# Kernel optimization log

Hardware: AMD Instinct MI355X
Metric: run time of the kernel (lower is better)

## Reference

```python
import jax, jax.numpy as jnp
import numpy as np

NUM_HEADS = 12
HEAD_DIM = 64
MASKED_BIAS = -10000.0


def setup_inputs() -> dict:
    key = jax.random.key(0)
    k1, k2, k3 = jax.random.split(key, 3)
    B, S, D = 2, 2048, 768
    return {
        "hidden_states": jax.random.normal(k1, (B, S, D), dtype=jnp.float32),
        "c_attn_w": jax.random.normal(k2, (D, 3 * D), dtype=jnp.float32) * 0.02,
        "c_attn_b": jnp.zeros((3 * D,), dtype=jnp.float32),
        "c_proj_w": jax.random.normal(k3, (D, D), dtype=jnp.float32) * 0.02,
        "c_proj_b": jnp.zeros((D,), dtype=jnp.float32),
    }


def _split_heads(x, B, S):
    # [B,S,D] -> [B,H,S,hd]
    return x.reshape(B, S, NUM_HEADS, HEAD_DIM).transpose(0, 2, 1, 3)


def reference(hidden_states, c_attn_w, c_attn_b, c_proj_w, c_proj_b):
    B, S, D = hidden_states.shape
    qkv = hidden_states @ c_attn_w + c_attn_b  # [B,S,3D]
    q, k, v = jnp.split(qkv, 3, axis=-1)
    q = _split_heads(q, B, S)
    k = _split_heads(k, B, S)
    v = _split_heads(v, B, S)

    # Unfused attention: full [B,H,S,S] scores, where-based causal mask
    attn_weights = jnp.einsum("bhqd,bhkd->bhqk", q, k)
    attn_weights = attn_weights / jnp.float32(HEAD_DIM) ** 0.5
    causal_mask = jnp.tril(jnp.ones((S, S), dtype=bool))[None, None]
    attn_weights = jnp.where(causal_mask, attn_weights,
                             jnp.asarray(MASKED_BIAS, attn_weights.dtype))
    attn_weights = jax.nn.softmax(attn_weights, axis=-1)
    attn_output = jnp.einsum("bhqk,bhkd->bhqd", attn_weights, v)

    # merge heads [B,H,S,hd] -> [B,S,D]
    attn_output = attn_output.transpose(0, 2, 1, 3).reshape(B, S, D)
    attn_output = attn_output @ c_proj_w + c_proj_b
    return attn_output
```

## Files before the change

### kernel.cpp

```cpp
#include <hip/hip_runtime.h>
#include <stdint.h>


constexpr int B_  = 2;
constexpr int S_  = 2048;
constexpr int D_  = 768;
constexpr int N3D = 3 * D_;
constexpr int M_  = B_ * S_;
constexpr int NTILE = 32 * 24;
#define QSCALE 0.1803368801111f
#define FIXED_M 8.0f

typedef __bf16 bv8 __attribute__((ext_vector_type(8)));
typedef float  fv4 __attribute__((ext_vector_type(4)));
typedef unsigned short uv4 __attribute__((ext_vector_type(4)));
typedef unsigned short uv8 __attribute__((ext_vector_type(8)));

__device__ inline unsigned short f2bf(float x) {
    __bf16 b = (__bf16)x;
    return __builtin_bit_cast(unsigned short, b);
}

__device__ inline fv4 mfma16(bv8 a, bv8 b, fv4 c) {
    return __builtin_amdgcn_mfma_f32_16x16x32_bf16(a, b, c, 0, 0, 0);
}

#define GLOAD_LDS16(g, l)                                                        \
    __builtin_amdgcn_global_load_lds(                                            \
        (__attribute__((address_space(1))) void*)(g),                            \
        (__attribute__((address_space(3))) void*)(l), 16, 0, 0)

#define VMCNT4() asm volatile("s_waitcnt vmcnt(4)" ::: "memory")
#define VMCNT0() asm volatile("s_waitcnt vmcnt(0)" ::: "memory")
#define BAR()                                                                    \
    do { asm volatile("" ::: "memory"); __builtin_amdgcn_s_barrier();            \
         asm volatile("" ::: "memory"); } while (0)

__global__ __launch_bounds__(256)
void prep(const float* __restrict__ hs, const float* __restrict__ wqkv,
          const float* __restrict__ wproj, unsigned short* __restrict__ hsb,
          unsigned short* __restrict__ wqkvT, unsigned short* __restrict__ wprojT,
          int* __restrict__ cnt)
{
    __shared__ float tl[32][33];
    const int bid = blockIdx.x, t = threadIdx.x;
    if (bid == 0 && t == 0) *cnt = 0;

    if (bid < 1536) {
        const size_t i = ((size_t)bid * 256 + t) * 8;
        const float4 a = *(const float4*)&hs[i];
        const float4 b = *(const float4*)&hs[i + 4];
        uv8 o;
        o[0] = f2bf(a.x); o[1] = f2bf(a.y); o[2] = f2bf(a.z); o[3] = f2bf(a.w);
        o[4] = f2bf(b.x); o[5] = f2bf(b.y); o[6] = f2bf(b.z); o[7] = f2bf(b.w);
        *(uv8*)&hsb[i] = o;
        return;
    }

    const float* W;
    unsigned short* WT;
    int K, N, bx, by;
    if (bid < 3264) {
        W = wqkv; WT = wqkvT; K = 768; N = 2304;
        const int b2 = bid - 1536; bx = b2 % 72; by = b2 / 72;
    } else {
        W = wproj; WT = wprojT; K = 768; N = 768;
        const int b2 = bid - 3264; bx = b2 % 24; by = b2 / 24;
    }
    const int n0 = bx * 32, k0 = by * 32;
    {
        const int r = t >> 3, c = (t & 7) * 4;
        const float4 v = *(const float4*)&W[(size_t)(k0 + r) * N + n0 + c];
        tl[r][c + 0] = v.x; tl[r][c + 1] = v.y; tl[r][c + 2] = v.z; tl[r][c + 3] = v.w;
    }
    __syncthreads();
    {
        const int rn = t >> 3, ck = (t & 7) * 4;
        uv4 o;
        o[0] = f2bf(tl[ck + 0][rn]); o[1] = f2bf(tl[ck + 1][rn]);
        o[2] = f2bf(tl[ck + 2][rn]); o[3] = f2bf(tl[ck + 3][rn]);
        *(uv4*)&WT[(size_t)(n0 + rn) * K + k0 + ck] = o;
    }
}

template<bool QKV>
__global__ __launch_bounds__(256)
void gemm_bf16(const unsigned short* __restrict__ A, const unsigned short* __restrict__ BT,
               const float* __restrict__ bias, float* __restrict__ Cf,
               unsigned short* __restrict__ Qb, unsigned short* __restrict__ Kb,
               unsigned short* __restrict__ VTb, int M, int N, int K)
{
    __shared__ unsigned short smem[16384];
    unsigned short* const sA0 = smem;
    unsigned short* const sB0 = smem + 8192;

    const int t = threadIdx.x, w = t >> 6, lane = t & 63;
    const int l15 = lane & 15, l4 = lane >> 4;
    const int m0 = blockIdx.y * 128, n0 = blockIdx.x * 128;
    const int wr = w >> 1, wc = w & 1;

    fv4 acc[4][4];
#pragma unroll
    for (int i = 0; i < 4; ++i)
#pragma unroll
        for (int j = 0; j < 4; ++j) acc[i][j] = fv4{0.f, 0.f, 0.f, 0.f};

    const int r0 = w * 16 + (lane >> 2);
    const int c0 = (lane & 3) ^ ((r0 >> 1) & 3);
    const int r1 = (w + 4) * 16 + (lane >> 2);
    const int c1 = (lane & 3) ^ ((r1 >> 1) & 3);

    auto stage = [&](int buf, int k0) {
        GLOAD_LDS16(A  + (size_t)(m0 + r0) * K + k0 + c0 * 8, sA0 + buf * 4096 + w * 512);
        GLOAD_LDS16(A  + (size_t)(m0 + r1) * K + k0 + c1 * 8, sA0 + buf * 4096 + (w + 4) * 512);
        GLOAD_LDS16(BT + (size_t)(n0 + r0) * K + k0 + c0 * 8, sB0 + buf * 4096 + w * 512);
        GLOAD_LDS16(BT + (size_t)(n0 + r1) * K + k0 + c1 * 8, sB0 + buf * 4096 + (w + 4) * 512);
    };

    stage(0, 0);
    const int nt = K >> 5;
    for (int tt = 0; tt < nt; ++tt) {
        const int cur = tt & 1;
        if (tt + 1 < nt) { stage(cur ^ 1, (tt + 1) * 32); VMCNT4(); }
        else             { VMCNT0(); }
        BAR();

        bv8 af[4], bf[4];
#pragma unroll
        for (int i = 0; i < 4; ++i) {
            const int r = wr * 64 + i * 16 + l15;
            const int c = l4 ^ ((r >> 1) & 3);
            af[i] = *(const bv8*)&sA0[cur * 4096 + r * 32 + c * 8];
        }
#pragma unroll
        for (int j = 0; j < 4; ++j) {
            const int r = wc * 64 + j * 16 + l15;
            const int c = l4 ^ ((r >> 1) & 3);
            bf[j] = *(const bv8*)&sB0[cur * 4096 + r * 32 + c * 8];
        }
        __builtin_amdgcn_s_setprio(1);
#pragma unroll
        for (int i = 0; i < 4; ++i)
#pragma unroll
            for (int j = 0; j < 4; ++j)
                acc[i][j] = mfma16(af[i], bf[j], acc[i][j]);
        __builtin_amdgcn_s_setprio(0);
        BAR();
    }

    if (QKV) {
        const int sect = n0 / 768;
        const int rem0 = n0 - sect * 768;
        if (sect < 2) {
            const float qs = (sect == 0) ? QSCALE : 1.0f;
#pragma unroll
            for (int jf = 0; jf < 4; ++jf) {
                const int c = wc * 64 + jf * 16 + l15;
                const float bb = bias[n0 + c];
                const int ch = c >> 3, off = c & 7;
#pragma unroll
                for (int i = 0; i < 4; ++i) {
                    const int rb = wr * 64 + i * 16 + l4 * 4;
#pragma unroll
                    for (int reg = 0; reg < 4; ++reg) {
                        const int r = rb + reg;
                        smem[r * 128 + ((ch ^ (r & 15)) << 3) + off] =
                            f2bf((acc[i][jf][reg] + bb) * qs);
                    }
                }
            }
            __syncthreads();
            unsigned short* const dstQK = (sect == 0) ? Qb : Kb;
            const int brow = m0 >> 11, sbase = m0 & 2047, hb = rem0 >> 6;
#pragma unroll
            for (int u = 0; u < 8; ++u) {
                const int ID = t + 256 * u;
                const int s = ID >> 4, ch = ID & 15;
                const int hh = ch >> 3, dc = ch & 7;
                const uv8 v = *(const uv8*)&smem[s * 128 + ((ch ^ (s & 15)) << 3)];
                const size_t bh = (size_t)brow * 12 + hb + hh;
                *(uv8*)&dstQK[(bh * 2048 + sbase + s) * 64 + dc * 8] = v;
            }
        } else {
#pragma unroll
            for (int jf = 0; jf < 4; ++jf) {
                const int col = n0 + wc * 64 + jf * 16 + l15;
                const float bb = bias[col];
                const int rem = col - 2 * 768;
                const int hh_ = rem >> 6, d = rem & 63;
#pragma unroll
                for (int i = 0; i < 4; ++i) {
                    const int rowb = m0 + wr * 64 + i * 16 + l4 * 4;
                    const size_t bh = (size_t)(rowb >> 11) * 12 + hh_;
                    const int s0 = rowb & 2047;
                    uv4 pk;
#pragma unroll
                    for (int reg = 0; reg < 4; ++reg) pk[reg] = f2bf(acc[i][jf][reg] + bb);
                    *(uv4*)&VTb[(bh * 64 + d) * 2048 + s0] = pk;
                }
            }
        }
    } else {
#pragma unroll
        for (int jf = 0; jf < 4; ++jf) {
            const int col = n0 + wc * 64 + jf * 16 + l15;
            const float bb = bias[col];
#pragma unroll
            for (int i = 0; i < 4; ++i) {
                const int rowb = m0 + wr * 64 + i * 16 + l4 * 4;
#pragma unroll
                for (int reg = 0; reg < 4; ++reg)
                    Cf[(size_t)(rowb + reg) * N + col] = acc[i][jf][reg] + bb;
            }
        }
    }
}

__global__ __launch_bounds__(256)
void flash_mfma(const unsigned short* __restrict__ Qb, const unsigned short* __restrict__ Kb,
                const unsigned short* __restrict__ VTb, unsigned short* __restrict__ outb,
                int* __restrict__ cnt)
{
    __shared__ unsigned short sK [2][64 * 64];
    __shared__ unsigned short sVT[2][64 * 64];
    __shared__ unsigned short sP [4][16 * 64];
    __shared__ int sj;

    const int t = threadIdx.x, w = t >> 6, lane = t & 63;
    const int l15 = lane & 15, l4 = lane >> 4;

    const int sr0 = w * 8 + (lane >> 3), sc0 = (lane & 7) ^ (sr0 & 7);
    const int sr1 = (w + 4) * 8 + (lane >> 3), sc1 = (lane & 7) ^ (sr1 & 7);

    for (;;) {
        if (t == 0) sj = atomicAdd(cnt, 1);
        __syncthreads();
        const int j = sj;
        if (j >= NTILE) return;
        const int qt = 31 - j / 24;
        const int bh = j - (j / 24) * 24;
        const int b = bh / 12, h = bh - b * 12;
        const int qrow = qt * 64 + w * 16;

        const unsigned short* Kbase = Kb  + (size_t)bh * 2048 * 64;
        const unsigned short* Vbase = VTb + (size_t)bh * 64 * 2048;

        bv8 qf[2];
        {
            const unsigned short* qp = Qb + ((size_t)bh * 2048 + qrow + l15) * 64 + l4 * 8;
            qf[0] = *(const bv8*)qp;
            qf[1] = *(const bv8*)(qp + 32);
        }

        fv4 o[4];
#pragma unroll
        for (int jf = 0; jf < 4; ++jf) o[jf] = fv4{0.f, 0.f, 0.f, 0.f};
        float l_ = 0.f;

        GLOAD_LDS16(Kbase + (size_t)sr0 * 64 + sc0 * 8, &sK[0][w * 512]);
        GLOAD_LDS16(Kbase + (size_t)sr1 * 64 + sc1 * 8, &sK[0][(w + 4) * 512]);
        GLOAD_LDS16(Vbase + (size_t)sr0 * 2048 + sc0 * 8, &sVT[0][w * 512]);
        GLOAD_LDS16(Vbase + (size_t)sr1 * 2048 + sc1 * 8, &sVT[0][(w + 4) * 512]);

        for (int kt = 0; kt <= qt; ++kt) {
            const int cur = kt & 1;
            if (kt < qt) {
                const int nk = kt + 1;
                GLOAD_LDS16(Kbase + (size_t)(nk * 64 + sr0) * 64 + sc0 * 8, &sK[cur ^ 1][w * 512]);
                GLOAD_LDS16(Kbase + (size_t)(nk * 64 + sr1) * 64 + sc1 * 8, &sK[cur ^ 1][(w + 4) * 512]);
                GLOAD_LDS16(Vbase + (size_t)sr0 * 2048 + nk * 64 + sc0 * 8, &sVT[cur ^ 1][w * 512]);
                GLOAD_LDS16(Vbase + (size_t)sr1 * 2048 + nk * 64 + sc1 * 8, &sVT[cur ^ 1][(w + 4) * 512]);
                VMCNT4();
            } else VMCNT0();
            BAR();

            fv4 st[4];
            __builtin_amdgcn_s_setprio(1);
#pragma unroll
            for (int jf = 0; jf < 4; ++jf) {
                st[jf] = fv4{-FIXED_M, -FIXED_M, -FIXED_M, -FIXED_M};
                const int kr = jf * 16 + l15;
#pragma unroll
                for (int hh = 0; hh < 2; ++hh) {
                    const bv8 ka = *(const bv8*)&sK[cur][kr * 64 + (((hh * 4 + l4) ^ (kr & 7)) * 8)];
                    st[jf] = mfma16(ka, qf[hh], st[jf]);
                }
            }
            __builtin_amdgcn_s_setprio(0);

            float ps[16];
            const int qg = qrow + l15;
            if (kt == qt) {
#pragma unroll
                for (int jf = 0; jf < 4; ++jf)
#pragma unroll
                    for (int reg = 0; reg < 4; ++reg) {
                        const int kvg = kt * 64 + jf * 16 + l4 * 4 + reg;
                        ps[jf * 4 + reg] = (kvg > qg) ? -30000.f : st[jf][reg];
                    }
            } else {
#pragma unroll
                for (int jf = 0; jf < 4; ++jf)
#pragma unroll
                    for (int reg = 0; reg < 4; ++reg) ps[jf * 4 + reg] = st[jf][reg];
            }
#pragma unroll
            for (int u = 0; u < 16; ++u) {
                const float p = exp2f(ps[u]);
                ps[u] = p;
                l_ += p;
            }

#pragma unroll
            for (int jf = 0; jf < 4; ++jf) {
                uv4 pk;
#pragma unroll
                for (int reg = 0; reg < 4; ++reg) pk[reg] = f2bf(ps[jf * 4 + reg]);
                const int chunk = jf * 2 + (l4 >> 1);
                *(uv4*)&sP[w][l15 * 64 + ((chunk ^ (l15 & 7)) * 8) + (l4 & 1) * 4] = pk;
            }

            bv8 pa[2];
#pragma unroll
            for (int hh = 0; hh < 2; ++hh)
                pa[hh] = *(const bv8*)&sP[w][l15 * 64 + (((hh * 4 + l4) ^ (l15 & 7)) * 8)];
            __builtin_amdgcn_s_setprio(1);
#pragma unroll
            for (int jf = 0; jf < 4; ++jf) {
                const int dr = jf * 16 + l15;
#pragma unroll
                for (int hh = 0; hh < 2; ++hh) {
                    const bv8 vb = *(const bv8*)&sVT[cur][dr * 64 + (((hh * 4 + l4) ^ (dr & 7)) * 8)];
                    o[jf] = mfma16(pa[hh], vb, o[jf]);
                }
            }
            __builtin_amdgcn_s_setprio(0);
            BAR();
        }

        l_ += __shfl_xor(l_, 16);
        l_ += __shfl_xor(l_, 32);
        const float inv = 1.0f / l_;
        float invq[4];
#pragma unroll
        for (int reg = 0; reg < 4; ++reg) invq[reg] = __shfl(inv, l4 * 4 + reg);
#pragma unroll
        for (int jf = 0; jf < 4; ++jf)
#pragma unroll
            for (int reg = 0; reg < 4; ++reg)
                outb[(size_t)(b * S_ + qrow + l4 * 4 + reg) * D_ + h * 64 + jf * 16 + l15] =
                    f2bf(o[jf][reg] * invq[reg]);
    }
}

extern "C" void kernel_launch(void* const* d_in, const int* in_sizes, int n_in,
                              void* d_out, int out_size, void* d_ws, size_t ws_size,
                              hipStream_t stream)
{
    const float* hs    = (const float*)d_in[0];
    const float* wqkv  = (const float*)d_in[1];
    const float* bqkv  = (const float*)d_in[2];
    const float* wproj = (const float*)d_in[3];
    const float* bproj = (const float*)d_in[4];
    float* out = (float*)d_out;

    unsigned short* hsb    = (unsigned short*)d_ws;
    unsigned short* wqkvT  = hsb    + (size_t)M_ * D_;
    unsigned short* wprojT = wqkvT  + (size_t)N3D * D_;
    unsigned short* Qb     = wprojT + (size_t)D_ * D_;
    unsigned short* Kb     = Qb     + (size_t)24 * 2048 * 64;
    unsigned short* VTb    = Kb     + (size_t)24 * 2048 * 64;
    unsigned short* attnb  = VTb    + (size_t)24 * 2048 * 64;
    int* cnt = (int*)(attnb + (size_t)M_ * D_);

    prep<<<3840, 256, 0, stream>>>(hs, wqkv, wproj, hsb, wqkvT, wprojT, cnt);
    gemm_bf16<true><<<dim3(N3D / 128, M_ / 128), 256, 0, stream>>>(
        hsb, wqkvT, bqkv, nullptr, Qb, Kb, VTb, M_, N3D, D_);
    flash_mfma<<<512, 256, 0, stream>>>(Qb, Kb, VTb, attnb, cnt);
    gemm_bf16<false><<<dim3(D_ / 128, M_ / 128), 256, 0, stream>>>(
        attnb, wprojT, bproj, out, nullptr, nullptr, nullptr, M_, D_, D_);
}
```

Measured before the change: 170.9 us.

## Split long causal attention tiles across two workgroups and triple-buffer GEMM loads

Query tiles 16-31 are split into two KV ranges handled by separate workgroups. The partial O and l values are combined through a global scratch buffer that reuses the hs bf16 region, using an atomic flag handshake with spin-wait. The change also moves the QKV/proj GEMMs to a 3-stage LDS pipeline, raises the flash grid from 512 to 768 persistent blocks, and splits the exp-sum into four accumulators. The aim is to balance the uneven causal workload and hide GEMM load latency, at the cost of more LDS per block, extra scratch traffic and a spin-wait that could stall if the partner block is not resident.

```diff
diff --git a/kernel.cpp b/kernel.cpp
--- a/kernel.cpp
+++ b/kernel.cpp
@@ -7,7 +7,7 @@
 constexpr int D_  = 768;
 constexpr int N3D = 3 * D_;
 constexpr int M_  = B_ * S_;
-constexpr int NTILE = 32 * 24;
+constexpr int NCHUNK = 1152;
 #define QSCALE 0.1803368801111f
 #define FIXED_M 8.0f
 
@@ -30,6 +30,7 @@
         (__attribute__((address_space(1))) void*)(g),                            \
         (__attribute__((address_space(3))) void*)(l), 16, 0, 0)
 
+#define VMCNT8() asm volatile("s_waitcnt vmcnt(8)" ::: "memory")
 #define VMCNT4() asm volatile("s_waitcnt vmcnt(4)" ::: "memory")
 #define VMCNT0() asm volatile("s_waitcnt vmcnt(0)" ::: "memory")
 #define BAR()                                                                    \
@@ -44,7 +45,9 @@
 {
     __shared__ float tl[32][33];
     const int bid = blockIdx.x, t = threadIdx.x;
-    if (bid == 0 && t == 0) *cnt = 0;
+    if (bid == 0) {
+        for (int i = t; i < 388; i += 256) cnt[i] = 0;
+    }
 
     if (bid < 1536) {
         const size_t i = ((size_t)bid * 256 + t) * 8;
@@ -90,9 +93,9 @@
                unsigned short* __restrict__ Qb, unsigned short* __restrict__ Kb,
                unsigned short* __restrict__ VTb, int M, int N, int K)
 {
-    __shared__ unsigned short smem[16384];
+    __shared__ unsigned short smem[24576];
     unsigned short* const sA0 = smem;
-    unsigned short* const sB0 = smem + 8192;
+    unsigned short* const sB0 = smem + 12288;
 
     const int t = threadIdx.x, w = t >> 6, lane = t & 63;
     const int l15 = lane & 15, l4 = lane >> 4;
@@ -118,11 +121,13 @@
     };
 
     stage(0, 0);
+    stage(1, 32);
     const int nt = K >> 5;
+    int cur = 0, sb = 2;
     for (int tt = 0; tt < nt; ++tt) {
-        const int cur = tt & 1;
-        if (tt + 1 < nt) { stage(cur ^ 1, (tt + 1) * 32); VMCNT4(); }
-        else             { VMCNT0(); }
+        if (tt + 2 < nt) { stage(sb, (tt + 2) * 32); sb = (sb == 2) ? 0 : sb + 1; VMCNT8(); }
+        else if (tt + 1 < nt) VMCNT4();
+        else VMCNT0();
         BAR();
 
         bv8 af[4], bf[4];
@@ -146,6 +151,7 @@
                 acc[i][j] = mfma16(af[i], bf[j], acc[i][j]);
         __builtin_amdgcn_s_setprio(0);
         BAR();
+        cur = (cur == 2) ? 0 : cur + 1;
     }
 
     if (QKV) {
@@ -219,12 +225,13 @@
 __global__ __launch_bounds__(256)
 void flash_mfma(const unsigned short* __restrict__ Qb, const unsigned short* __restrict__ Kb,
                 const unsigned short* __restrict__ VTb, unsigned short* __restrict__ outb,
-                int* __restrict__ cnt)
+                int* __restrict__ cnt, int* __restrict__ flags,
+                float* __restrict__ scrO, float* __restrict__ scrL)
 {
     __shared__ unsigned short sK [2][64 * 64];
     __shared__ unsigned short sVT[2][64 * 64];
     __shared__ unsigned short sP [4][16 * 64];
-    __shared__ int sj;
+    __shared__ int sComm;
 
     const int t = threadIdx.x, w = t >> 6, lane = t & 63;
     const int l15 = lane & 15, l4 = lane >> 4;
@@ -233,12 +240,22 @@
     const int sr1 = (w + 4) * 8 + (lane >> 3), sc1 = (lane & 7) ^ (sr1 & 7);
 
     for (;;) {
-        if (t == 0) sj = atomicAdd(cnt, 1);
+        if (t == 0) sComm = atomicAdd(cnt, 1);
         __syncthreads();
-        const int j = sj;
-        if (j >= NTILE) return;
-        const int qt = 31 - j / 24;
-        const int bh = j - (j / 24) * 24;
+        const int j = sComm;
+        if (j >= NCHUNK) return;
+
+        const int tier = j / 24;
+        const int bh = j - tier * 24;
+        int qt, k0, k1, split;
+        if (tier < 16)       { qt = 31 - tier; k0 = 0;  k1 = 15; split = 1; }
+        else if (tier == 16) { qt = 31;        k0 = 16; k1 = 31; split = 1; }
+        else if (tier == 17) { qt = 15;        k0 = 0;  k1 = 15; split = 0; }
+        else {
+            const int u = tier - 18, s = 15 - (u >> 1);
+            if ((u & 1) == 0) { qt = 15 + s; k0 = 16; k1 = qt; split = 1; }
+            else              { qt = s - 1;  k0 = 0;  k1 = qt; split = 0; }
+        }
         const int b = bh / 12, h = bh - b * 12;
         const int qrow = qt * 64 + w * 16;
 
@@ -257,14 +274,14 @@
         for (int jf = 0; jf < 4; ++jf) o[jf] = fv4{0.f, 0.f, 0.f, 0.f};
         float l_ = 0.f;
 
-        GLOAD_LDS16(Kbase + (size_t)sr0 * 64 + sc0 * 8, &sK[0][w * 512]);
-        GLOAD_LDS16(Kbase + (size_t)sr1 * 64 + sc1 * 8, &sK[0][(w + 4) * 512]);
-        GLOAD_LDS16(Vbase + (size_t)sr0 * 2048 + sc0 * 8, &sVT[0][w * 512]);
-        GLOAD_LDS16(Vbase + (size_t)sr1 * 2048 + sc1 * 8, &sVT[0][(w + 4) * 512]);
-
-        for (int kt = 0; kt <= qt; ++kt) {
-            const int cur = kt & 1;
-            if (kt < qt) {
+        GLOAD_LDS16(Kbase + (size_t)(k0 * 64 + sr0) * 64 + sc0 * 8, &sK[0][w * 512]);
+        GLOAD_LDS16(Kbase + (size_t)(k0 * 64 + sr1) * 64 + sc1 * 8, &sK[0][(w + 4) * 512]);
+        GLOAD_LDS16(Vbase + (size_t)sr0 * 2048 + k0 * 64 + sc0 * 8, &sVT[0][w * 512]);
+        GLOAD_LDS16(Vbase + (size_t)sr1 * 2048 + k0 * 64 + sc1 * 8, &sVT[0][(w + 4) * 512]);
+
+        for (int kt = k0; kt <= k1; ++kt) {
+            const int cur = (kt - k0) & 1;
+            if (kt < k1) {
                 const int nk = kt + 1;
                 GLOAD_LDS16(Kbase + (size_t)(nk * 64 + sr0) * 64 + sc0 * 8, &sK[cur ^ 1][w * 512]);
                 GLOAD_LDS16(Kbase + (size_t)(nk * 64 + sr1) * 64 + sc1 * 8, &sK[cur ^ 1][(w + 4) * 512]);
@@ -304,12 +321,15 @@
 #pragma unroll
                     for (int reg = 0; reg < 4; ++reg) ps[jf * 4 + reg] = st[jf][reg];
             }
-#pragma unroll
-            for (int u = 0; u < 16; ++u) {
-                const float p = exp2f(ps[u]);
-                ps[u] = p;
-                l_ += p;
-            }
+            float la0 = 0.f, la1 = 0.f, la2 = 0.f, la3 = 0.f;
+#pragma unroll
+            for (int u = 0; u < 16; u += 4) {
+                const float p0 = exp2f(ps[u + 0]); ps[u + 0] = p0; la0 += p0;
+                const float p1 = exp2f(ps[u + 1]); ps[u + 1] = p1; la1 += p1;
+                const float p2 = exp2f(ps[u + 2]); ps[u + 2] = p2; la2 += p2;
+                const float p3 = exp2f(ps[u + 3]); ps[u + 3] = p3; la3 += p3;
+            }
+            l_ += (la0 + la1) + (la2 + la3);
 
 #pragma unroll
             for (int jf = 0; jf < 4; ++jf) {
@@ -340,16 +360,62 @@
 
         l_ += __shfl_xor(l_, 16);
         l_ += __shfl_xor(l_, 32);
-        const float inv = 1.0f / l_;
-        float invq[4];
-#pragma unroll
-        for (int reg = 0; reg < 4; ++reg) invq[reg] = __shfl(inv, l4 * 4 + reg);
-#pragma unroll
-        for (int jf = 0; jf < 4; ++jf)
-#pragma unroll
-            for (int reg = 0; reg < 4; ++reg)
-                outb[(size_t)(b * S_ + qrow + l4 * 4 + reg) * D_ + h * 64 + jf * 16 + l15] =
-                    f2bf(o[jf][reg] * invq[reg]);
+
+        if (!split) {
+            const float inv = 1.0f / l_;
+            float invq[4];
+#pragma unroll
+            for (int reg = 0; reg < 4; ++reg) invq[reg] = __shfl(inv, l4 * 4 + reg);
+#pragma unroll
+            for (int jf = 0; jf < 4; ++jf)
+#pragma unroll
+                for (int reg = 0; reg < 4; ++reg)
+                    outb[(size_t)(b * S_ + qrow + l4 * 4 + reg) * D_ + h * 64 + jf * 16 + l15] =
+                        f2bf(o[jf][reg] * invq[reg]);
+        } else {
+            const int pair = (qt - 16) * 24 + bh;
+            if (t == 0)
+                sComm = __hip_atomic_fetch_add(&flags[pair], 1, __ATOMIC_RELAXED,
+                                               __HIP_MEMORY_SCOPE_AGENT);
+            __syncthreads();
+            const int old = sComm;
+            if (old == 0) {
+#pragma unroll
+                for (int jf = 0; jf < 4; ++jf)
+#pragma unroll
+                    for (int reg = 0; reg < 4; ++reg)
+                        scrO[(size_t)pair * 4096 + (w * 16 + l4 * 4 + reg) * 64 + jf * 16 + l15] =
+                            o[jf][reg];
+                if (l4 == 0) scrL[pair * 64 + w * 16 + l15] = l_;
+                __threadfence();
+                __syncthreads();
+                if (t == 0)
+                    __hip_atomic_fetch_add(&flags[pair], 2, __ATOMIC_RELEASE,
+                                           __HIP_MEMORY_SCOPE_AGENT);
+            } else {
+                if (t == 0) {
+                    while (__hip_atomic_load(&flags[pair], __ATOMIC_ACQUIRE,
+                                             __HIP_MEMORY_SCOPE_AGENT) < 4)
+                        __builtin_amdgcn_s_sleep(2);
+                }
+                __syncthreads();
+                __threadfence();
+                const float lo = scrL[pair * 64 + w * 16 + l15];
+                const float inv = 1.0f / (l_ + lo);
+                float invq[4];
+#pragma unroll
+                for (int reg = 0; reg < 4; ++reg) invq[reg] = __shfl(inv, l4 * 4 + reg);
+#pragma unroll
+                for (int jf = 0; jf < 4; ++jf)
+#pragma unroll
+                    for (int reg = 0; reg < 4; ++reg) {
+                        const float ov =
+                            scrO[(size_t)pair * 4096 + (w * 16 + l4 * 4 + reg) * 64 + jf * 16 + l15];
+                        outb[(size_t)(b * S_ + qrow + l4 * 4 + reg) * D_ + h * 64 + jf * 16 + l15] =
+                            f2bf((o[jf][reg] + ov) * invq[reg]);
+                    }
+            }
+        }
     }
 }
 
@@ -371,12 +437,15 @@
     unsigned short* Kb     = Qb     + (size_t)24 * 2048 * 64;
     unsigned short* VTb    = Kb     + (size_t)24 * 2048 * 64;
     unsigned short* attnb  = VTb    + (size_t)24 * 2048 * 64;
-    int* cnt = (int*)(attnb + (size_t)M_ * D_);
+    int*   cnt   = (int*)(attnb + (size_t)M_ * D_);
+    int*   flags = cnt + 4;
+    float* scrL  = (float*)(flags + 384);
+    float* scrO  = (float*)hsb;
 
     prep<<<3840, 256, 0, stream>>>(hs, wqkv, wproj, hsb, wqkvT, wprojT, cnt);
     gemm_bf16<true><<<dim3(N3D / 128, M_ / 128), 256, 0, stream>>>(
         hsb, wqkvT, bqkv, nullptr, Qb, Kb, VTb, M_, N3D, D_);
-    flash_mfma<<<512, 256, 0, stream>>>(Qb, Kb, VTb, attnb, cnt);
+    flash_mfma<<<768, 256, 0, stream>>>(Qb, Kb, VTb, attnb, cnt, flags, scrO, scrL);
     gemm_bf16<false><<<dim3(D_ / 128, M_ / 128), 256, 0, stream>>>(
         attnb, wprojT, bproj, out, nullptr, nullptr, nullptr, M_, D_, D_);
 }
```

Result: slower. 276.3 us (+61.7%).
